# Kernel optimization log

Hardware: AMD Instinct MI355X
Metric: run time of the kernel (lower is better)

The kernel has to match this reference:

```python
import jax, jax.numpy as jnp
import numpy as np

B, T, D = 1, 2048, 4096
N_HEADS, KV_HEADS, HEAD_DIM = 32, 8, 128
WINDOW = 1024
ROPE_THETA = 500000.0
EPS = 1e-6
LARGE_NEGATIVE = np.finfo(np.float32).min


def _rms_norm(x, w, eps=EPS):
    xf = x.astype(jnp.float32)
    out = xf * jax.lax.rsqrt(jnp.square(xf).mean(-1, keepdims=True) + eps)
    return (w.astype(jnp.float32) * out).astype(x.dtype)


def _positions_from_segment_ids(seg_ids):
    t = seg_ids.shape[1]
    return jax.vmap(lambda row: jnp.where(row != 0, jnp.arange(t) - jnp.argmax(row), 2 ** 30))(seg_ids)


def _rope_sin_cos(positions, head_dim=HEAD_DIM, theta=ROPE_THETA):
    fraction = jnp.arange(0, head_dim, 2, dtype=jnp.float32) / head_dim
    inv_freq = 1.0 / (theta ** fraction)
    sinusoid = jnp.einsum('BT,k->BTk', positions.astype(jnp.float32), inv_freq)
    return jnp.sin(sinusoid), jnp.cos(sinusoid)


def _apply_rope(x, sin, cos):
    half = x.shape[-1] // 2
    x1, x2 = x[..., :half], x[..., half:]
    sin, cos = sin[:, :, None, :], cos[:, :, None, :]
    return jnp.concatenate([x1 * cos - x2 * sin, x2 * cos + x1 * sin], axis=-1).astype(x.dtype)


def setup_inputs() -> dict:
    key = jax.random.key(0)
    ks = jax.random.split(key, 6)
    wscale = 1.0 / np.sqrt(D)
    return {
        'x': jax.random.normal(ks[0], (B, T, D), dtype=jnp.float32),
        'Wq': jax.random.normal(ks[1], (D, N_HEADS * HEAD_DIM), dtype=jnp.float32) * wscale,
        'Wk': jax.random.normal(ks[2], (D, KV_HEADS * HEAD_DIM), dtype=jnp.float32) * wscale,
        'Wv': jax.random.normal(ks[3], (D, KV_HEADS * HEAD_DIM), dtype=jnp.float32) * wscale,
        'Wo': jax.random.normal(ks[4], (N_HEADS * HEAD_DIM, D), dtype=jnp.float32) * wscale,
        'q_norm_w': jnp.ones((N_HEADS * HEAD_DIM,), dtype=jnp.float32),
        'k_norm_w': jnp.ones((KV_HEADS * HEAD_DIM,), dtype=jnp.float32),
        'segment_ids': jnp.ones((B, T), dtype=jnp.int32),
    }


def reference(x, Wq, Wk, Wv, Wo, q_norm_w, k_norm_w, segment_ids):
    b, t, _ = x.shape
    positions = _positions_from_segment_ids(segment_ids)
    sin, cos = _rope_sin_cos(positions)

    # QKV projections; q/k RMS-normed over the flattened (heads*head_dim) axis pre-reshape.
    q = _rms_norm(x @ Wq, q_norm_w).reshape(b, t, N_HEADS, HEAD_DIM)
    k = _rms_norm(x @ Wk, k_norm_w).reshape(b, t, KV_HEADS, HEAD_DIM)
    v = (x @ Wv).reshape(b, t, KV_HEADS, HEAD_DIM)

    q = _apply_rope(q, sin, cos)
    k = _apply_rope(k, sin, cos)

    # GQA: physically repeat kv heads (repeat_kv in source).
    n_rep = N_HEADS // KV_HEADS
    k = jnp.repeat(k[:, :, :, None, :], n_rep, axis=3).reshape(b, t, N_HEADS, HEAD_DIM)
    v = jnp.repeat(v[:, :, :, None, :], n_rep, axis=3).reshape(b, t, N_HEADS, HEAD_DIM)

    # causal + sliding-window + same-segment mask, [B, T, S]
    i = positions[:, :, None]
    j = positions[:, None, :]
    same_seg = segment_ids[:, :, None] == segment_ids[:, None, :]
    mask = (j <= i) & ((i - j) < WINDOW) & same_seg & (segment_ids != 0)[:, None, :]

    scale = HEAD_DIM ** -0.5
    logits = jnp.einsum('BTNH,BSNH->BNTS', q, k) * jnp.array(scale, dtype=q.dtype)
    padded = jnp.where(mask[:, None, :, :], logits.astype(jnp.float32), LARGE_NEGATIVE)
    probs = jax.nn.softmax(padded, axis=-1).astype(k.dtype)
    attn = jnp.einsum('BNTS,BSNH->BTNH', probs, v)
    return attn.reshape(b, t, N_HEADS * HEAD_DIM) @ Wo
```

## Files before the change

kernel.cpp:

```cpp
#include <hip/hip_runtime.h>
#include <cstdint>
#include <cstddef>

typedef __bf16 bf16_t;
typedef __bf16 bf16x8 __attribute__((ext_vector_type(8)));
typedef __bf16 bf16x4 __attribute__((ext_vector_type(4)));
typedef __bf16 bf16x2 __attribute__((ext_vector_type(2)));
typedef float f32x4 __attribute__((ext_vector_type(4)));

#define T_LEN 2048
#define DMODEL 4096
#define NHEADS 32
#define KVHEADS 8
#define HD 128
#define QD 4096
#define KD 1024
#define QKVD 6144
#define WIN 1024
#define VS 72
#define WMAX 1152

__global__ void pos_kernel(const int* __restrict__ seg, int* __restrict__ positions) {
  __shared__ int svals[256], sidx[256];
  int tid = threadIdx.x;
  int bestv = -2147483647 - 1, besti = 0;
  for (int t = tid; t < T_LEN; t += 256) {
    int v = seg[t];
    if (v > bestv) { bestv = v; besti = t; }
  }
  svals[tid] = bestv; sidx[tid] = besti;
  __syncthreads();
  for (int st = 128; st > 0; st >>= 1) {
    if (tid < st) {
      if (svals[tid+st] > svals[tid] || (svals[tid+st] == svals[tid] && sidx[tid+st] < sidx[tid])) {
        svals[tid] = svals[tid+st]; sidx[tid] = sidx[tid+st];
      }
    }
    __syncthreads();
  }
  int amax = sidx[0];
  for (int t = tid; t < T_LEN; t += 256)
    positions[t] = (seg[t] != 0) ? (t - amax) : (1 << 30);
}

__global__ void sincos_kernel(const int* __restrict__ positions, float* __restrict__ sc) {
  int t = blockIdx.x, i = threadIdx.x;
  float inv = expf(-(float)i * (logf(500000.0f) / 64.0f));
  float ang = (float)positions[t] * inv;
  sc[(t*64 + i)*2 + 0] = sinf(ang);
  sc[(t*64 + i)*2 + 1] = cosf(ang);
}

__global__ void cvt_kernel(const float* __restrict__ in, bf16_t* __restrict__ out, int n) {
  int i = (blockIdx.x * blockDim.x + threadIdx.x) * 8;
  if (i >= n) return;
  float4 a = *(const float4*)(in + i);
  float4 b = *(const float4*)(in + i + 4);
  bf16x8 o;
  o[0]=(bf16_t)a.x; o[1]=(bf16_t)a.y; o[2]=(bf16_t)a.z; o[3]=(bf16_t)a.w;
  o[4]=(bf16_t)b.x; o[5]=(bf16_t)b.y; o[6]=(bf16_t)b.z; o[7]=(bf16_t)b.w;
  *(bf16x8*)(out + i) = o;
}

__global__ void transcvt_kernel(const float* __restrict__ W, bf16_t* __restrict__ Wt, int K, int N) {
  __shared__ float tile[32][33];
  int tx = threadIdx.x, ty = threadIdx.y;
  int bx = blockIdx.x, by = blockIdx.y;
  #pragma unroll
  for (int i = 0; i < 4; i++) {
    int k = by*32 + ty + i*8;
    tile[ty + i*8][tx] = W[(size_t)k * N + bx*32 + tx];
  }
  __syncthreads();
  int t = ty*32 + tx;
  int n = t >> 3;
  int kq = t & 7;
  bf16x4 v;
  #pragma unroll
  for (int e = 0; e < 4; e++) v[e] = (bf16_t)tile[kq*4 + e][n];
  *(bf16x4*)(Wt + (size_t)(bx*32 + n) * K + by*32 + kq*4) = v;
}

__device__ __forceinline__ void gld_lds16(const void* g, void* l) {
  __builtin_amdgcn_global_load_lds((__attribute__((address_space(1))) void*)g,
                                   (__attribute__((address_space(3))) void*)l, 16, 0, 0);
}

__global__ __launch_bounds__(512, 2) void gemm1_kernel(
    const bf16_t* __restrict__ A, const bf16_t* __restrict__ Bt,
    bf16_t* __restrict__ Cb, int M, int N, int K, int NBM) {
  __shared__ bf16_t As[2 * 128 * 64];
  __shared__ bf16_t Bs[2 * 192 * 64];
  int tid = threadIdx.x;
  int w = tid >> 6, l = tid & 63, lr = l & 15, lg = l >> 4;
  int wr = w >> 2, wc = w & 3;
  int nwg = gridDim.x;
  int wg  = blockIdx.x;
  int cpx = nwg >> 3;
  int swz = (wg & 7) * cpx + (wg >> 3);
  int bm = swz % NBM, bn = swz / NBM;
  const int NT = K >> 6;

  auto stageA = [&](int tt, int h) {
    bf16_t* ldsb = As + (tt & 1)*8192 + h*4096;
    int row = tid >> 3;
    int scn = (tid & 7) ^ (row & 7);
    gld_lds16(A + ((size_t)bm*128 + h*64 + row) * K + tt*64 + scn*8,
              ldsb + w*512);
  };
  auto stageB = [&](int tt, int u) {
    bf16_t* ldsb = Bs + (tt & 1)*12288 + u*4096;
    int row = tid >> 3;
    int scn = (tid & 7) ^ (row & 7);
    gld_lds16(Bt + ((size_t)bn*192 + u*64 + row) * K + tt*64 + scn*8,
              ldsb + w*512);
  };
  auto afrag = [&](int b2, int row, int kk) -> bf16x8 {
    int chunk = (kk*4 + lg) ^ (row & 7);
    return *(const bf16x8*)((const char*)(As + b2*8192) + row*128 + chunk*16);
  };
  auto bfrag = [&](int b2, int row, int kk) -> bf16x8 {
    int chunk = (kk*4 + lg) ^ (row & 7);
    return *(const bf16x8*)((const char*)(Bs + b2*12288) + row*128 + chunk*16);
  };

  f32x4 acc[4][3] = {};
  bf16x8 a[4][2], bb[3][2];

  stageA(0, 0); stageA(0, 1); stageB(0, 0); stageB(0, 1); stageB(0, 2);
  stageA(1, 0); stageA(1, 1); stageB(1, 0); stageB(1, 1);
  asm volatile("s_waitcnt vmcnt(4)" ::: "memory");
  __builtin_amdgcn_s_barrier();

  for (int t = 0; t < NT; t++) {
    int b = t & 1;
    #pragma unroll
    for (int fm = 0; fm < 4; fm++)
      #pragma unroll
      for (int kk = 0; kk < 2; kk++)
        a[fm][kk] = afrag(b, wr*64 + fm*16 + lr, kk);
    #pragma unroll
    for (int kk = 0; kk < 2; kk++)
      bb[0][kk] = bfrag(b, wc*48 + lr, kk);
    if (t + 1 < NT) stageB(t + 1, 2);
    __builtin_amdgcn_s_barrier();
    asm volatile("s_waitcnt lgkmcnt(0)" ::: "memory");
    __builtin_amdgcn_s_setprio(1);
    #pragma unroll
    for (int fm = 0; fm < 4; fm++)
      #pragma unroll
      for (int kk = 0; kk < 2; kk++)
        acc[fm][0] = __builtin_amdgcn_mfma_f32_16x16x32_bf16(a[fm][kk], bb[0][kk], acc[fm][0], 0, 0, 0);
    __builtin_amdgcn_s_setprio(0);
    __builtin_amdgcn_s_barrier();
    #pragma unroll
    for (int kk = 0; kk < 2; kk++)
      bb[1][kk] = bfrag(b, wc*48 + 16 + lr, kk);
    if (t + 2 < NT) { stageA(t + 2, 0); stageA(t + 2, 1); }
    __builtin_amdgcn_s_barrier();
    asm volatile("s_waitcnt lgkmcnt(0)" ::: "memory");
    __builtin_amdgcn_s_setprio(1);
    #pragma unroll
    for (int fm = 0; fm < 4; fm++)
      #pragma unroll
      for (int kk = 0; kk < 2; kk++)
        acc[fm][1] = __builtin_amdgcn_mfma_f32_16x16x32_bf16(a[fm][kk], bb[1][kk], acc[fm][1], 0, 0, 0);
    __builtin_amdgcn_s_setprio(0);
    __builtin_amdgcn_s_barrier();
    #pragma unroll
    for (int kk = 0; kk < 2; kk++)
      bb[2][kk] = bfrag(b, wc*48 + 32 + lr, kk);
    __builtin_amdgcn_s_barrier();
    asm volatile("s_waitcnt lgkmcnt(0)" ::: "memory");
    __builtin_amdgcn_s_setprio(1);
    #pragma unroll
    for (int fm = 0; fm < 4; fm++)
      acc[fm][2] = __builtin_amdgcn_mfma_f32_16x16x32_bf16(a[fm][0], bb[2][0], acc[fm][2], 0, 0, 0);
    __builtin_amdgcn_s_setprio(0);
    __builtin_amdgcn_s_barrier();
    if (t + 2 < NT) { stageB(t + 2, 0); stageB(t + 2, 1); }
    __builtin_amdgcn_s_setprio(1);
    #pragma unroll
    for (int fm = 0; fm < 4; fm++)
      acc[fm][2] = __builtin_amdgcn_mfma_f32_16x16x32_bf16(a[fm][1], bb[2][1], acc[fm][2], 0, 0, 0);
    __builtin_amdgcn_s_setprio(0);
    if (t < NT - 2) asm volatile("s_waitcnt vmcnt(4)" ::: "memory");
    else            asm volatile("s_waitcnt vmcnt(0)" ::: "memory");
    __builtin_amdgcn_s_barrier();
  }

  #pragma unroll
  for (int fm = 0; fm < 4; fm++) {
    #pragma unroll
    for (int fn = 0; fn < 3; fn++) {
      #pragma unroll
      for (int r2 = 0; r2 < 4; r2++) {
        int row = bm*128 + wr*64 + fm*16 + lg*4 + r2;
        int col = bn*192 + wc*48 + fn*16 + lr;
        Cb[(size_t)row * N + col] = (bf16_t)acc[fm][fn][r2];
      }
    }
  }
}

#define MFMA_QUAD(FM0, FN0)                                                     \
  { _Pragma("unroll") for (int fm_ = 0; fm_ < QFM; fm_++)                        \
    _Pragma("unroll") for (int fn_ = 0; fn_ < 2; fn_++)                          \
    _Pragma("unroll") for (int kk_ = 0; kk_ < 2; kk_++)                          \
      acc[(FM0)+fm_][(FN0)+fn_] = __builtin_amdgcn_mfma_f32_16x16x32_bf16(       \
          a[(FM0)+fm_][kk_], bb[(FN0)+fn_][kk_], acc[(FM0)+fm_][(FN0)+fn_], 0,0,0); }

template<bool WRITE_BF16, int AM>
__global__ __launch_bounds__(512, 2) void gemm256_kernel(
    const bf16_t* __restrict__ A, const bf16_t* __restrict__ Bt,
    bf16_t* __restrict__ Cb, float* __restrict__ Cf,
    int M, int N, int K, int NBM) {
  constexpr int BM  = AM * 128;
  constexpr int NH  = AM + 2;
  constexpr int FM2 = AM * 4;
  constexpr int QFM = AM * 2;
  __shared__ bf16_t As[2 * BM * 64];
  __shared__ bf16_t Bs[2 * 256 * 64];
  int tid = threadIdx.x;
  int w = tid >> 6, l = tid & 63, lr = l & 15, lg = l >> 4;
  int wr = w >> 2, wc = w & 3;
  int nwg = gridDim.x;
  int wg  = blockIdx.x;
  int cpx = nwg >> 3;
  int swz = (wg & 7) * cpx + (wg >> 3);
  int bm = swz % NBM, bn = swz / NBM;
  const int NT = K >> 6;

  auto stage = [&](int tt, int h) {
    int b2 = tt & 1;
    const bf16_t* G; size_t grow0; bf16_t* ldsb;
    if (h < AM) { G = A;  grow0 = (size_t)bm*BM + h*128;        ldsb = As + b2*(BM*64) + h*8192; }
    else        { G = Bt; grow0 = (size_t)bn*256 + (h-AM)*128;  ldsb = Bs + b2*16384 + (h-AM)*8192; }
    int kcol = tt * 64;
    #pragma unroll
    for (int r2 = 0; r2 < 2; r2++) {
      int L = r2*8192 + tid*16;
      int row = L >> 7;
      int chunk = (L >> 4) & 7;
      int scn = chunk ^ (row & 7);
      gld_lds16(G + (grow0 + (size_t)row) * K + kcol + scn*8,
                ldsb + r2*4096 + w*512);
    }
  };
  auto afrag = [&](int b2, int row, int kk) -> bf16x8 {
    int chunk = (kk*4 + lg) ^ (row & 7);
    return *(const bf16x8*)((const char*)(As + b2*(BM*64)) + row*128 + chunk*16);
  };
  auto bfrag = [&](int b2, int row, int kk) -> bf16x8 {
    int chunk = (kk*4 + lg) ^ (row & 7);
    return *(const bf16x8*)((const char*)(Bs + b2*16384) + row*128 + chunk*16);
  };

  f32x4 acc[FM2][4] = {};
  bf16x8 a[FM2][2], bb[4][2];

  #pragma unroll
  for (int h = 0; h < NH; h++) stage(0, h);
  #pragma unroll
  for (int h = 0; h < NH - 1; h++) stage(1, h);
  if constexpr (AM == 2) asm volatile("s_waitcnt vmcnt(6)" ::: "memory");
  else                   asm volatile("s_waitcnt vmcnt(4)" ::: "memory");
  __builtin_amdgcn_s_barrier();

  for (int t = 0; t < NT; t++) {
    int b = t & 1;
    #pragma unroll
    for (int fm = 0; fm < FM2; fm++)
      #pragma unroll
      for (int kk = 0; kk < 2; kk++)
        a[fm][kk] = afrag(b, wr*(BM/2) + fm*16 + lr, kk);
    #pragma unroll
    for (int fn = 0; fn < 2; fn++)
      #pragma unroll
      for (int kk = 0; kk < 2; kk++)
        bb[fn][kk] = bfrag(b, wc*64 + fn*16 + lr, kk);
    if (t + 1 < NT) stage(t + 1, NH - 1);
    __builtin_amdgcn_s_barrier();
    asm volatile("s_waitcnt lgkmcnt(0)" ::: "memory");
    __builtin_amdgcn_s_setprio(1);
    MFMA_QUAD(0, 0);
    __builtin_amdgcn_s_setprio(0);
    __builtin_amdgcn_s_barrier();
    #pragma unroll
    for (int fn = 2; fn < 4; fn++)
      #pragma unroll
      for (int kk = 0; kk < 2; kk++)
        bb[fn][kk] = bfrag(b, wc*64 + fn*16 + lr, kk);
    if (t + 2 < NT) stage(t + 2, 0);
    __builtin_amdgcn_s_barrier();
    asm volatile("s_waitcnt lgkmcnt(0)" ::: "memory");
    __builtin_amdgcn_s_setprio(1);
    MFMA_QUAD(0, 2);
    __builtin_amdgcn_s_setprio(0);
    __builtin_amdgcn_s_barrier();
    if (t + 2 < NT) stage(t + 2, 1);
    __builtin_amdgcn_s_barrier();
    __builtin_amdgcn_s_setprio(1);
    MFMA_QUAD(QFM, 2);
    __builtin_amdgcn_s_setprio(0);
    __builtin_amdgcn_s_barrier();
    if constexpr (AM == 2) { if (t + 2 < NT) stage(t + 2, 2); }
    __builtin_amdgcn_s_barrier();
    __builtin_amdgcn_s_setprio(1);
    MFMA_QUAD(QFM, 0);
    __builtin_amdgcn_s_setprio(0);
    if (t < NT - 2) {
      if constexpr (AM == 2) asm volatile("s_waitcnt vmcnt(6)" ::: "memory");
      else                   asm volatile("s_waitcnt vmcnt(4)" ::: "memory");
    } else {
      asm volatile("s_waitcnt vmcnt(0)" ::: "memory");
    }
    __builtin_amdgcn_s_barrier();
  }

  #pragma unroll
  for (int fm = 0; fm < FM2; fm++) {
    #pragma unroll
    for (int fn = 0; fn < 4; fn++) {
      #pragma unroll
      for (int r2 = 0; r2 < 4; r2++) {
        int row = bm*BM + wr*(BM/2) + fm*16 + lg*4 + r2;
        int col = bn*256 + wc*64 + fn*16 + lr;
        if (WRITE_BF16) Cb[(size_t)row * N + col] = (bf16_t)acc[fm][fn][r2];
        else            Cf[(size_t)row * N + col] = acc[fm][fn][r2];
      }
    }
  }
}

__global__ __launch_bounds__(256) void normrope_kernel(bf16_t* __restrict__ qkv,
    const float* __restrict__ qw, const float* __restrict__ kw,
    const float* __restrict__ sc) {
  int t = blockIdx.x;
  int tid = threadIdx.x;
  bf16_t* qrow = qkv + (size_t)t * QKVD;
  bf16_t* krow = qrow + QD;
  __shared__ float red[8];
  float s = 0.f;
  {
    const bf16x8* p = (const bf16x8*)(qrow + tid*16);
    bf16x8 v0 = p[0], v1 = p[1];
    #pragma unroll
    for (int j = 0; j < 8; j++) { float a = (float)v0[j], b = (float)v1[j]; s += a*a + b*b; }
  }
  #pragma unroll
  for (int o = 32; o; o >>= 1) s += __shfl_xor(s, o);
  if ((tid & 63) == 0) red[tid >> 6] = s;
  float sk = 0.f;
  {
    bf16x4 v = *(const bf16x4*)(krow + tid*4);
    #pragma unroll
    for (int j = 0; j < 4; j++) { float a = (float)v[j]; sk += a*a; }
  }
  #pragma unroll
  for (int o = 32; o; o >>= 1) sk += __shfl_xor(sk, o);
  if ((tid & 63) == 0) red[4 + (tid >> 6)] = sk;
  __syncthreads();
  float rq = rsqrtf((red[0]+red[1]+red[2]+red[3]) / (float)QD + 1e-6f);
  float rk = rsqrtf((red[4]+red[5]+red[6]+red[7]) / (float)KD + 1e-6f);
  const float ascale = 0.08838834764831845f;
  for (int p = tid; p < 2048; p += 256) {
    int hh = p >> 6, i = p & 63;
    int i1 = hh*HD + i, i2 = i1 + 64;
    float x1 = (float)qrow[i1] * rq * qw[i1];
    float x2 = (float)qrow[i2] * rq * qw[i2];
    float sn = sc[(t*64 + i)*2 + 0], cs = sc[(t*64 + i)*2 + 1];
    qrow[i1] = (bf16_t)((x1*cs - x2*sn) * ascale);
    qrow[i2] = (bf16_t)((x2*cs + x1*sn) * ascale);
  }
  for (int p = tid; p < 512; p += 256) {
    int hh = p >> 6, i = p & 63;
    int i1 = hh*HD + i, i2 = i1 + 64;
    float x1 = (float)krow[i1] * rk * kw[i1];
    float x2 = (float)krow[i2] * rk * kw[i2];
    float sn = sc[(t*64 + i)*2 + 0], cs = sc[(t*64 + i)*2 + 1];
    krow[i1] = (bf16_t)(x1*cs - x2*sn);
    krow[i2] = (bf16_t)(x2*cs + x1*sn);
  }
}

__global__ __launch_bounds__(512, 3) void attn_kernel(const bf16_t* __restrict__ qkv,
    const int* __restrict__ positions, const int* __restrict__ seg,
    bf16_t* __restrict__ O) {
  __shared__ bf16_t Ks[2][64 * HD];
  __shared__ bf16_t Vt[HD * VS];
  __shared__ bf16_t P[8][16 * VS];
  __shared__ int posL[WMAX];
  __shared__ int segL[WMAX];
  int tid = threadIdx.x;
  int w = tid >> 6, l = tid & 63, lr = l & 15, lg = l >> 4;
  int qb = (gridDim.x - 1 - blockIdx.x) * 128;
  int h = blockIdx.y;
  int kvh = h >> 2;
  int q0 = qb + w * 16;
  const bf16_t* Kg = qkv + QD + (size_t)kvh * HD;
  const bf16_t* Vg = qkv + QD + KD + (size_t)kvh * HD;

  bf16x8 qf[4];
  {
    const bf16_t* Qrow = qkv + (size_t)(q0 + lr) * QKVD + h * HD;
    #pragma unroll
    for (int c = 0; c < 4; c++) qf[c] = *(const bf16x8*)(Qrow + c*32 + lg*8);
  }
  int pos_i[4], seg_i[4];
  #pragma unroll
  for (int r = 0; r < 4; r++) { int i = q0 + lg*4 + r; pos_i[r] = positions[i]; seg_i[r] = seg[i]; }
  f32x4 o[8] = {};
  float m[4], lsum[4];
  #pragma unroll
  for (int r = 0; r < 4; r++) { m[r] = -__builtin_inff(); lsum[r] = 0.f; }

  int vkp = tid & 31, vdg = tid >> 5;
  bf16x8 vrA, vrB;

  auto issueK = [&](int j0, int buf) {
    #pragma unroll
    for (int i = 0; i < 2; i++) {
      int c = tid + i*512;
      int row = c >> 4;
      int scn = (c & 15) ^ (row & 7);
      gld_lds16(Kg + (size_t)(j0 + row) * QKVD + scn*8,
                (char*)Ks[buf] + (size_t)(i*512 + (tid & 448))*16);
    }
  };
  auto loadV = [&](int j0) {
    const bf16_t* vp = Vg + (size_t)(j0 + 2*vkp) * QKVD + vdg*8;
    vrA = *(const bf16x8*)vp;
    vrB = *(const bf16x8*)(vp + QKVD);
  };

  int jstart = qb - (WIN - 1); if (jstart < 0) jstart = 0; jstart &= ~63;
  const int jlast = qb + 64;
  const int wlen = qb + 128 - jstart;
  loadV(jstart);
  issueK(jstart, 0);
  for (int i = tid; i < wlen; i += 512) {
    posL[i] = positions[jstart + i];
    segL[i] = seg[jstart + i];
  }
  asm volatile("s_waitcnt lgkmcnt(0)" ::: "memory");
  __builtin_amdgcn_s_barrier();

  int nt = 0;
  for (int j0 = jstart; j0 <= jlast; j0 += 64, nt++) {
    int b = nt & 1;
    bool hasNext = (j0 + 64 <= jlast);
    #pragma unroll
    for (int e = 0; e < 8; e++) {
      bf16x2 pr; pr[0] = vrA[e]; pr[1] = vrB[e];
      *(bf16x2*)(Vt + (vdg*8 + e)*VS + 2*vkp) = pr;
    }
    int pj[4], sj[4];
    #pragma unroll
    for (int kt = 0; kt < 4; kt++) {
      int ji = j0 - jstart + kt*16 + lr;
      pj[kt] = posL[ji]; sj[kt] = segL[ji];
    }
    asm volatile("" ::: "memory");
    if (hasNext) { loadV(j0 + 64); issueK(j0 + 64, b ^ 1); }
    asm volatile("" ::: "memory");
    if (hasNext) asm volatile("s_waitcnt vmcnt(4) lgkmcnt(0)" ::: "memory");
    else         asm volatile("s_waitcnt vmcnt(0) lgkmcnt(0)" ::: "memory");
    __builtin_amdgcn_s_barrier();

    bool active = (j0 <= q0 + 15) && (j0 + 63 >= q0 - (WIN - 1));
    if (active) {
      f32x4 s[4] = {};
      __builtin_amdgcn_s_setprio(1);
      #pragma unroll
      for (int kt = 0; kt < 4; kt++) {
        int row = kt*16 + lr;
        const char* kb = (const char*)Ks[b] + row*256;
        #pragma unroll
        for (int c = 0; c < 4; c++) {
          bf16x8 kf = *(const bf16x8*)(kb + (((c*4 + lg) ^ (row & 7)) * 16));
          s[kt] = __builtin_amdgcn_mfma_f32_16x16x32_bf16(qf[c], kf, s[kt], 0, 0, 0);
        }
      }
      __builtin_amdgcn_s_setprio(0);
      #pragma unroll
      for (int kt = 0; kt < 4; kt++) {
        #pragma unroll
        for (int r = 0; r < 4; r++) {
          bool valid = (pj[kt] <= pos_i[r]) && (pos_i[r] - pj[kt] < WIN) && (seg_i[r] == sj[kt]) && (sj[kt] != 0);
          s[kt][r] = valid ? s[kt][r] : -__builtin_inff();
        }
      }
      #pragma unroll
      for (int r = 0; r < 4; r++) {
        float smax = fmaxf(fmaxf(s[0][r], s[1][r]), fmaxf(s[2][r], s[3][r]));
        if (__any(smax > m[r] + 8.f)) {
          float rm = smax;
          #pragma unroll
          for (int o2 = 1; o2 < 16; o2 <<= 1) rm = fmaxf(rm, __shfl_xor(rm, o2));
          if (rm > m[r] + 8.f) {
            float rescale = __expf(m[r] - rm);
            lsum[r] *= rescale;
            #pragma unroll
            for (int n = 0; n < 8; n++) o[n][r] *= rescale;
            m[r] = rm;
          }
        }
        float mub = fmaxf(m[r], -1e37f);
        float p0 = __expf(s[0][r] - mub);
        float p1 = __expf(s[1][r] - mub);
        float p2 = __expf(s[2][r] - mub);
        float p3 = __expf(s[3][r] - mub);
        lsum[r] += (p0 + p1) + (p2 + p3);
        int prow = (lg*4 + r) * VS;
        P[w][prow + lr]      = (bf16_t)p0;
        P[w][prow + 16 + lr] = (bf16_t)p1;
        P[w][prow + 32 + lr] = (bf16_t)p2;
        P[w][prow + 48 + lr] = (bf16_t)p3;
      }
      __builtin_amdgcn_s_setprio(1);
      #pragma unroll
      for (int ks = 0; ks < 2; ks++) {
        bf16x8 pa = *(const bf16x8*)(&P[w][lr*VS + ks*32 + lg*8]);
        #pragma unroll
        for (int n = 0; n < 8; n++) {
          bf16x8 vb = *(const bf16x8*)(&Vt[(n*16 + lr)*VS + ks*32 + lg*8]);
          o[n] = __builtin_amdgcn_mfma_f32_16x16x32_bf16(pa, vb, o[n], 0, 0, 0);
        }
      }
      __builtin_amdgcn_s_setprio(0);
    }
    __builtin_amdgcn_s_barrier();
  }
  #pragma unroll
  for (int r = 0; r < 4; r++) {
    float ls = lsum[r];
    #pragma unroll
    for (int o2 = 1; o2 < 16; o2 <<= 1) ls += __shfl_xor(ls, o2);
    float inv = ls > 0.f ? 1.f / ls : 0.f;
    int row = q0 + lg*4 + r;
    #pragma unroll
    for (int n = 0; n < 8; n++)
      O[(size_t)row * QD + h*HD + n*16 + lr] = (bf16_t)(o[n][r] * inv);
  }
}

extern "C" void kernel_launch(void* const* d_in, const int* in_sizes, int n_in,
                              void* d_out, int out_size, void* d_ws, size_t ws_size,
                              hipStream_t stream) {
  (void)in_sizes; (void)n_in; (void)out_size; (void)ws_size;
  const float* x  = (const float*)d_in[0];
  const float* Wq = (const float*)d_in[1];
  const float* Wk = (const float*)d_in[2];
  const float* Wv = (const float*)d_in[3];
  const float* Wo = (const float*)d_in[4];
  const float* qw = (const float*)d_in[5];
  const float* kw = (const float*)d_in[6];
  const int*  seg = (const int*)d_in[7];
  float* out = (float*)d_out;

  char* base = (char*)d_ws;
  size_t off = 0;
  auto alloc = [&](size_t b) { void* r = base + off; off = (off + b + 255) & ~(size_t)255; return r; };
  bf16_t* xb    = (bf16_t*)alloc((size_t)T_LEN * DMODEL * 2);
  bf16_t* Wallt = (bf16_t*)alloc((size_t)QKVD * DMODEL * 2);
  bf16_t* Wot   = (bf16_t*)alloc((size_t)DMODEL * QD * 2);
  bf16_t* qkv   = (bf16_t*)alloc((size_t)T_LEN * QKVD * 2);
  int*    posi  = (int*)alloc((size_t)T_LEN * 4);
  float*  sc    = (float*)alloc((size_t)T_LEN * 64 * 2 * 4);
  bf16_t* ao    = xb;

  pos_kernel<<<1, 256, 0, stream>>>(seg, posi);
  sincos_kernel<<<T_LEN, 64, 0, stream>>>(posi, sc);
  cvt_kernel<<<(T_LEN * DMODEL / 8 + 255) / 256, 256, 0, stream>>>(x, xb, T_LEN * DMODEL);
  transcvt_kernel<<<dim3(QD/32, DMODEL/32), dim3(32, 8), 0, stream>>>(Wq, Wallt, DMODEL, QD);
  transcvt_kernel<<<dim3(KD/32, DMODEL/32), dim3(32, 8), 0, stream>>>(Wk, Wallt + (size_t)QD * DMODEL, DMODEL, KD);
  transcvt_kernel<<<dim3(KD/32, DMODEL/32), dim3(32, 8), 0, stream>>>(Wv, Wallt + (size_t)(QD + KD) * DMODEL, DMODEL, KD);
  transcvt_kernel<<<dim3(DMODEL/32, QD/32), dim3(32, 8), 0, stream>>>(Wo, Wot, QD, DMODEL);
  gemm1_kernel<<<dim3((T_LEN/128)*(QKVD/192)), 512, 0, stream>>>(
      xb, Wallt, qkv, T_LEN, QKVD, DMODEL, T_LEN/128);
  normrope_kernel<<<T_LEN, 256, 0, stream>>>(qkv, qw, kw, sc);
  attn_kernel<<<dim3(T_LEN/128, NHEADS), 512, 0, stream>>>(qkv, posi, seg, ao);
  gemm256_kernel<false, 1><<<dim3((T_LEN/128)*(DMODEL/256)), 512, 0, stream>>>(
      ao, Wot, nullptr, out, T_LEN, DMODEL, QD, T_LEN/128);
}
```

Before: 356.6 us.

## Process 32 query rows per wave in attention, halving block threads

The attention kernel now runs 4 waves of 256 threads, each handling two 16-row query groups (32 rows), instead of 8 waves each handling 16 rows. Each K fragment and V fragment read from LDS now feeds two MFMAs, which cuts LDS traffic per FLOP and raises MFMA density. Loads of K/V tiles are split across fewer threads, so each thread issues twice as many loads. Register pressure doubles for accumulators, which lowers occupancy (launch bounds now 256,2), and the causal early-exit granularity becomes coarser.

Measured after the change: 337.8 us. -5.3%, faster.

```diff
diff --git a/kernel.cpp b/kernel.cpp
--- a/kernel.cpp
+++ b/kernel.cpp
@@ -384,12 +384,12 @@
   }
 }
 
-__global__ __launch_bounds__(512, 3) void attn_kernel(const bf16_t* __restrict__ qkv,
+__global__ __launch_bounds__(256, 2) void attn_kernel(const bf16_t* __restrict__ qkv,
     const int* __restrict__ positions, const int* __restrict__ seg,
     bf16_t* __restrict__ O) {
   __shared__ bf16_t Ks[2][64 * HD];
   __shared__ bf16_t Vt[HD * VS];
-  __shared__ bf16_t P[8][16 * VS];
+  __shared__ bf16_t P[4][32 * VS];
   __shared__ int posL[WMAX];
   __shared__ int segL[WMAX];
   int tid = threadIdx.x;
@@ -397,41 +397,54 @@
   int qb = (gridDim.x - 1 - blockIdx.x) * 128;
   int h = blockIdx.y;
   int kvh = h >> 2;
-  int q0 = qb + w * 16;
+  int q0 = qb + w * 32;
   const bf16_t* Kg = qkv + QD + (size_t)kvh * HD;
   const bf16_t* Vg = qkv + QD + KD + (size_t)kvh * HD;
 
-  bf16x8 qf[4];
-  {
-    const bf16_t* Qrow = qkv + (size_t)(q0 + lr) * QKVD + h * HD;
-    #pragma unroll
-    for (int c = 0; c < 4; c++) qf[c] = *(const bf16x8*)(Qrow + c*32 + lg*8);
-  }
-  int pos_i[4], seg_i[4];
-  #pragma unroll
-  for (int r = 0; r < 4; r++) { int i = q0 + lg*4 + r; pos_i[r] = positions[i]; seg_i[r] = seg[i]; }
-  f32x4 o[8] = {};
-  float m[4], lsum[4];
-  #pragma unroll
-  for (int r = 0; r < 4; r++) { m[r] = -__builtin_inff(); lsum[r] = 0.f; }
-
-  int vkp = tid & 31, vdg = tid >> 5;
-  bf16x8 vrA, vrB;
+  bf16x8 qf[2][4];
+  #pragma unroll
+  for (int g = 0; g < 2; g++) {
+    const bf16_t* Qrow = qkv + (size_t)(q0 + g*16 + lr) * QKVD + h * HD;
+    #pragma unroll
+    for (int c = 0; c < 4; c++) qf[g][c] = *(const bf16x8*)(Qrow + c*32 + lg*8);
+  }
+  int pos_i[2][4], seg_i[2][4];
+  #pragma unroll
+  for (int g = 0; g < 2; g++)
+    #pragma unroll
+    for (int r = 0; r < 4; r++) {
+      int i = q0 + g*16 + lg*4 + r;
+      pos_i[g][r] = positions[i]; seg_i[g][r] = seg[i];
+    }
+  f32x4 o[2][8] = {};
+  float m[2][4], lsum[2][4];
+  #pragma unroll
+  for (int g = 0; g < 2; g++)
+    #pragma unroll
+    for (int r = 0; r < 4; r++) { m[g][r] = -__builtin_inff(); lsum[g][r] = 0.f; }
+
+  int vkp[2], vdg[2];
+  #pragma unroll
+  for (int si = 0; si < 2; si++) { int item = tid + si*256; vkp[si] = item & 31; vdg[si] = item >> 5; }
+  bf16x8 vrA[2], vrB[2];
 
   auto issueK = [&](int j0, int buf) {
     #pragma unroll
-    for (int i = 0; i < 2; i++) {
-      int c = tid + i*512;
+    for (int i = 0; i < 4; i++) {
+      int c = tid + i*256;
       int row = c >> 4;
       int scn = (c & 15) ^ (row & 7);
       gld_lds16(Kg + (size_t)(j0 + row) * QKVD + scn*8,
-                (char*)Ks[buf] + (size_t)(i*512 + (tid & 448))*16);
+                (char*)Ks[buf] + (size_t)(i*256 + (tid & 192))*16);
     }
   };
   auto loadV = [&](int j0) {
-    const bf16_t* vp = Vg + (size_t)(j0 + 2*vkp) * QKVD + vdg*8;
-    vrA = *(const bf16x8*)vp;
-    vrB = *(const bf16x8*)(vp + QKVD);
+    #pragma unroll
+    for (int si = 0; si < 2; si++) {
+      const bf16_t* vp = Vg + (size_t)(j0 + 2*vkp[si]) * QKVD + vdg[si]*8;
+      vrA[si] = *(const bf16x8*)vp;
+      vrB[si] = *(const bf16x8*)(vp + QKVD);
+    }
   };
 
   int jstart = qb - (WIN - 1); if (jstart < 0) jstart = 0; jstart &= ~63;
@@ -439,7 +452,7 @@
   const int wlen = qb + 128 - jstart;
   loadV(jstart);
   issueK(jstart, 0);
-  for (int i = tid; i < wlen; i += 512) {
+  for (int i = tid; i < wlen; i += 256) {
     posL[i] = positions[jstart + i];
     segL[i] = seg[jstart + i];
   }
@@ -451,9 +464,12 @@
     int b = nt & 1;
     bool hasNext = (j0 + 64 <= jlast);
     #pragma unroll
-    for (int e = 0; e < 8; e++) {
-      bf16x2 pr; pr[0] = vrA[e]; pr[1] = vrB[e];
-      *(bf16x2*)(Vt + (vdg*8 + e)*VS + 2*vkp) = pr;
+    for (int si = 0; si < 2; si++) {
+      #pragma unroll
+      for (int e = 0; e < 8; e++) {
+        bf16x2 pr; pr[0] = vrA[si][e]; pr[1] = vrB[si][e];
+        *(bf16x2*)(Vt + (vdg[si]*8 + e)*VS + 2*vkp[si]) = pr;
+      }
     }
     int pj[4], sj[4];
     #pragma unroll
@@ -464,13 +480,13 @@
     asm volatile("" ::: "memory");
     if (hasNext) { loadV(j0 + 64); issueK(j0 + 64, b ^ 1); }
     asm volatile("" ::: "memory");
-    if (hasNext) asm volatile("s_waitcnt vmcnt(4) lgkmcnt(0)" ::: "memory");
+    if (hasNext) asm volatile("s_waitcnt vmcnt(8) lgkmcnt(0)" ::: "memory");
     else         asm volatile("s_waitcnt vmcnt(0) lgkmcnt(0)" ::: "memory");
     __builtin_amdgcn_s_barrier();
 
-    bool active = (j0 <= q0 + 15) && (j0 + 63 >= q0 - (WIN - 1));
+    bool active = (j0 <= q0 + 31) && (j0 + 63 >= q0 - (WIN - 1));
     if (active) {
-      f32x4 s[4] = {};
+      f32x4 s[2][4] = {};
       __builtin_amdgcn_s_setprio(1);
       #pragma unroll
       for (int kt = 0; kt < 4; kt++) {
@@ -479,53 +495,63 @@
         #pragma unroll
         for (int c = 0; c < 4; c++) {
           bf16x8 kf = *(const bf16x8*)(kb + (((c*4 + lg) ^ (row & 7)) * 16));
-          s[kt] = __builtin_amdgcn_mfma_f32_16x16x32_bf16(qf[c], kf, s[kt], 0, 0, 0);
+          #pragma unroll
+          for (int g = 0; g < 2; g++)
+            s[g][kt] = __builtin_amdgcn_mfma_f32_16x16x32_bf16(qf[g][c], kf, s[g][kt], 0, 0, 0);
         }
       }
       __builtin_amdgcn_s_setprio(0);
       #pragma unroll
-      for (int kt = 0; kt < 4; kt++) {
+      for (int kt = 0; kt < 4; kt++)
+        #pragma unroll
+        for (int g = 0; g < 2; g++)
+          #pragma unroll
+          for (int r = 0; r < 4; r++) {
+            bool valid = (pj[kt] <= pos_i[g][r]) && (pos_i[g][r] - pj[kt] < WIN) && (seg_i[g][r] == sj[kt]) && (sj[kt] != 0);
+            s[g][kt][r] = valid ? s[g][kt][r] : -__builtin_inff();
+          }
+      #pragma unroll
+      for (int g = 0; g < 2; g++)
         #pragma unroll
         for (int r = 0; r < 4; r++) {
-          bool valid = (pj[kt] <= pos_i[r]) && (pos_i[r] - pj[kt] < WIN) && (seg_i[r] == sj[kt]) && (sj[kt] != 0);
-          s[kt][r] = valid ? s[kt][r] : -__builtin_inff();
+          float smax = fmaxf(fmaxf(s[g][0][r], s[g][1][r]), fmaxf(s[g][2][r], s[g][3][r]));
+          if (__any(smax > m[g][r] + 8.f)) {
+            float rm = smax;
+            #pragma unroll
+            for (int o2 = 1; o2 < 16; o2 <<= 1) rm = fmaxf(rm, __shfl_xor(rm, o2));
+            if (rm > m[g][r] + 8.f) {
+              float rescale = __expf(m[g][r] - rm);
+              lsum[g][r] *= rescale;
+              #pragma unroll
+              for (int n = 0; n < 8; n++) o[g][n][r] *= rescale;
+              m[g][r] = rm;
+            }
+          }
+          float mub = fmaxf(m[g][r], -1e37f);
+          float p0 = __expf(s[g][0][r] - mub);
+          float p1 = __expf(s[g][1][r] - mub);
+          float p2 = __expf(s[g][2][r] - mub);
+          float p3 = __expf(s[g][3][r] - mub);
+          lsum[g][r] += (p0 + p1) + (p2 + p3);
+          int prow = (g*16 + lg*4 + r) * VS;
+          P[w][prow + lr]      = (bf16_t)p0;
+          P[w][prow + 16 + lr] = (bf16_t)p1;
+          P[w][prow + 32 + lr] = (bf16_t)p2;
+          P[w][prow + 48 + lr] = (bf16_t)p3;
         }
-      }
-      #pragma unroll
-      for (int r = 0; r < 4; r++) {
-        float smax = fmaxf(fmaxf(s[0][r], s[1][r]), fmaxf(s[2][r], s[3][r]));
-        if (__any(smax > m[r] + 8.f)) {
-          float rm = smax;
-          #pragma unroll
-          for (int o2 = 1; o2 < 16; o2 <<= 1) rm = fmaxf(rm, __shfl_xor(rm, o2));
-          if (rm > m[r] + 8.f) {
-            float rescale = __expf(m[r] - rm);
-            lsum[r] *= rescale;
-            #pragma unroll
-            for (int n = 0; n < 8; n++) o[n][r] *= rescale;
-            m[r] = rm;
-          }
-        }
-        float mub = fmaxf(m[r], -1e37f);
-        float p0 = __expf(s[0][r] - mub);
-        float p1 = __expf(s[1][r] - mub);
-        float p2 = __expf(s[2][r] - mub);
-        float p3 = __expf(s[3][r] - mub);
-        lsum[r] += (p0 + p1) + (p2 + p3);
-        int prow = (lg*4 + r) * VS;
-        P[w][prow + lr]      = (bf16_t)p0;
-        P[w][prow + 16 + lr] = (bf16_t)p1;
-        P[w][prow + 32 + lr] = (bf16_t)p2;
-        P[w][prow + 48 + lr] = (bf16_t)p3;
-      }
       __builtin_amdgcn_s_setprio(1);
       #pragma unroll
       for (int ks = 0; ks < 2; ks++) {
-        bf16x8 pa = *(const bf16x8*)(&P[w][lr*VS + ks*32 + lg*8]);
+        bf16x8 pa[2];
+        #pragma unroll
+        for (int g = 0; g < 2; g++)
+          pa[g] = *(const bf16x8*)(&P[w][(g*16 + lr)*VS + ks*32 + lg*8]);
         #pragma unroll
         for (int n = 0; n < 8; n++) {
           bf16x8 vb = *(const bf16x8*)(&Vt[(n*16 + lr)*VS + ks*32 + lg*8]);
-          o[n] = __builtin_amdgcn_mfma_f32_16x16x32_bf16(pa, vb, o[n], 0, 0, 0);
+          #pragma unroll
+          for (int g = 0; g < 2; g++)
+            o[g][n] = __builtin_amdgcn_mfma_f32_16x16x32_bf16(pa[g], vb, o[g][n], 0, 0, 0);
         }
       }
       __builtin_amdgcn_s_setprio(0);
@@ -533,16 +559,18 @@
     __builtin_amdgcn_s_barrier();
   }
   #pragma unroll
-  for (int r = 0; r < 4; r++) {
-    float ls = lsum[r];
-    #pragma unroll
-    for (int o2 = 1; o2 < 16; o2 <<= 1) ls += __shfl_xor(ls, o2);
-    float inv = ls > 0.f ? 1.f / ls : 0.f;
-    int row = q0 + lg*4 + r;
-    #pragma unroll
-    for (int n = 0; n < 8; n++)
-      O[(size_t)row * QD + h*HD + n*16 + lr] = (bf16_t)(o[n][r] * inv);
-  }
+  for (int g = 0; g < 2; g++)
+    #pragma unroll
+    for (int r = 0; r < 4; r++) {
+      float ls = lsum[g][r];
+      #pragma unroll
+      for (int o2 = 1; o2 < 16; o2 <<= 1) ls += __shfl_xor(ls, o2);
+      float inv = ls > 0.f ? 1.f / ls : 0.f;
+      int row = q0 + g*16 + lg*4 + r;
+      #pragma unroll
+      for (int n = 0; n < 8; n++)
+        O[(size_t)row * QD + h*HD + n*16 + lr] = (bf16_t)(o[g][n][r] * inv);
+    }
 }
 
 extern "C" void kernel_launch(void* const* d_in, const int* in_sizes, int n_in,
@@ -580,7 +608,7 @@
   gemm1_kernel<<<dim3((T_LEN/128)*(QKVD/192)), 512, 0, stream>>>(
       xb, Wallt, qkv, T_LEN, QKVD, DMODEL, T_LEN/128);
   normrope_kernel<<<T_LEN, 256, 0, stream>>>(qkv, qw, kw, sc);
-  attn_kernel<<<dim3(T_LEN/128, NHEADS), 512, 0, stream>>>(qkv, posi, seg, ao);
+  attn_kernel<<<dim3(T_LEN/128, NHEADS), 256, 0, stream>>>(qkv, posi, seg, ao);
   gemm256_kernel<false, 1><<<dim3((T_LEN/128)*(DMODEL/256)), 512, 0, stream>>>(
       ao, Wot, nullptr, out, T_LEN, DMODEL, QD, T_LEN/128);
 }
```
